# Kernel optimization log

Measured on AMD Instinct MI355X. Metric: run time of the kernel, lower is better.

## Reference

```python
import jax, jax.numpy as jnp
import numpy as np

GAMMA = 1.0
ALPHA = 0.5
EMBED_DIM = 256
N = 8192
M = 8192


def setup_inputs() -> dict:
    key = jax.random.key(0)
    k1, k2, k3, k4 = jax.random.split(key, 4)
    a = jax.random.normal(k1, (N, EMBED_DIM), dtype=jnp.float32)
    b = jax.random.normal(k2, (M, EMBED_DIM), dtype=jnp.float32)
    # torch.nn.Linear default init: U(-1/sqrt(fan_in), 1/sqrt(fan_in))
    lim = 1.0 / np.sqrt(EMBED_DIM)
    Wq = jax.random.uniform(k3, (EMBED_DIM, EMBED_DIM), jnp.float32, -lim, lim)
    Wk = jax.random.uniform(k4, (EMBED_DIM, EMBED_DIM), jnp.float32, -lim, lim)
    return {"a": a, "b": b, "Wq": Wq, "Wk": Wk}


def reference(a, b, Wq, Wk):
    # Vectorized Gram matrix of HybridKernelMethod.forward over all (a_i, b_j) pairs.
    inv_sqrt_d = np.float32(1.0 / np.sqrt(EMBED_DIM))
    ab = a @ b.T                                           # [N, M] cross dot products
    # RBF part: ||a_i - b_j||^2 = ||a_i||^2 + ||b_j||^2 - 2 a_i.b_j
    sq = (jnp.sum(a * a, axis=-1)[:, None]
          + jnp.sum(b * b, axis=-1)[None, :] - 2.0 * ab)
    rbf_sim = jnp.exp(-GAMMA * sq)                         # [N, M]
    # Attention part: per pair, q k^T is a 1x1 matrix, so softmax == 1 exactly.
    q = a @ Wq.T                                           # [N, D]
    k = b @ Wk.T                                           # [M, D]
    s = (q @ k.T) * inv_sqrt_d                             # [N, M] scores
    scores = jax.nn.softmax(s[..., None], axis=-1)[..., 0]  # all-ones, faithful to 1x1 softmax
    attn_sim = scores * ab                                 # sum((scores @ v) * x) == scores * (a.b)
    return (1.0 - ALPHA) * rbf_sim + ALPHA * attn_sim      # [N, M] Gram matrix
```

## Files before the change

kernel.cpp:

```cpp
#include <hip/hip_runtime.h>
#include <stdint.h>

#define DIM 256
#define NROWS 8192
#define OUTC 8192

#define BM 128
#define BN 128
#define BK 64

typedef __bf16 bf16x8_t __attribute__((ext_vector_type(8)));
typedef float f32x4_t __attribute__((ext_vector_type(4)));

__device__ __forceinline__ unsigned short f2bf_rne(float f) {
    unsigned int u = __float_as_uint(f);
    u += 0x7FFFu + ((u >> 16) & 1u);
    return (unsigned short)(u >> 16);
}

__global__ void prep_kernel(const float* __restrict__ src,
                            unsigned short* __restrict__ dst,
                            float* __restrict__ norms) {
    const int w = threadIdx.x >> 6;
    const int l = threadIdx.x & 63;
    const int row = blockIdx.x * 4 + w;
    const float4 v = reinterpret_cast<const float4*>(src + (size_t)row * DIM)[l];
    float ss = v.x * v.x + v.y * v.y + v.z * v.z + v.w * v.w;
#pragma unroll
    for (int off = 32; off > 0; off >>= 1) ss += __shfl_down(ss, off);
    if (l == 0) norms[row] = ss;
    ushort4 o = make_ushort4(f2bf_rne(v.x), f2bf_rne(v.y), f2bf_rne(v.z), f2bf_rne(v.w));
    reinterpret_cast<ushort4*>(dst + (size_t)row * DIM)[l] = o;
}

__global__ __launch_bounds__(256) void gemm_kernel(
        const unsigned short* __restrict__ aB,
        const unsigned short* __restrict__ bB,
        const float* __restrict__ na,
        const float* __restrict__ nb,
        float* __restrict__ out) {
    __shared__ unsigned short sA[BM * BK];
    __shared__ unsigned short sB[BN * BK];

    const int t = threadIdx.x;
    const int w = t >> 6;
    const int l = t & 63;
    const int wr = w >> 1;
    const int wc = w & 1;

    const int by = blockIdx.x >> 6;
    const int bx = blockIdx.x & 63;
    const int row0 = by * BM;
    const int col0 = bx * BN;

    f32x4_t acc[4][4];
#pragma unroll
    for (int m = 0; m < 4; ++m)
#pragma unroll
        for (int n = 0; n < 4; ++n) acc[m][n] = (f32x4_t)0.0f;

    const int lr = l >> 3;
    const int lc = (l & 7) * 8;
    const int fr = l & 15;
    const int kq = l >> 4;

#pragma unroll
    for (int kt = 0; kt < DIM / BK; ++kt) {
#pragma unroll
        for (int it = 0; it < 4; ++it) {
            const int rg = w * 4 + it;
            const int r = rg * 8 + lr;
            const unsigned short* ga = aB + (size_t)(row0 + r) * DIM + kt * BK + lc;
            const unsigned short* gb = bB + (size_t)(col0 + r) * DIM + kt * BK + lc;
            __builtin_amdgcn_global_load_lds(
                (const __attribute__((address_space(1))) void*)ga,
                (__attribute__((address_space(3))) void*)&sA[rg * 8 * BK], 16, 0, 0);
            __builtin_amdgcn_global_load_lds(
                (const __attribute__((address_space(1))) void*)gb,
                (__attribute__((address_space(3))) void*)&sB[rg * 8 * BK], 16, 0, 0);
        }
        __syncthreads();

#pragma unroll
        for (int ks = 0; ks < 2; ++ks) {
            bf16x8_t af[4], bfr[4];
#pragma unroll
            for (int m = 0; m < 4; ++m)
                af[m] = *reinterpret_cast<const bf16x8_t*>(
                    &sA[(wr * 64 + m * 16 + fr) * BK + ks * 32 + kq * 8]);
#pragma unroll
            for (int n = 0; n < 4; ++n)
                bfr[n] = *reinterpret_cast<const bf16x8_t*>(
                    &sB[(wc * 64 + n * 16 + fr) * BK + ks * 32 + kq * 8]);
#pragma unroll
            for (int m = 0; m < 4; ++m)
#pragma unroll
                for (int n = 0; n < 4; ++n)
                    acc[m][n] = __builtin_amdgcn_mfma_f32_16x16x32_bf16(
                        af[m], bfr[n], acc[m][n], 0, 0, 0);
        }
        __syncthreads();
    }

#pragma unroll
    for (int m = 0; m < 4; ++m) {
        const int rbase = row0 + wr * 64 + m * 16 + kq * 4;
#pragma unroll
        for (int q = 0; q < 4; ++q) {
            const int r = rbase + q;
            const float nar = na[r];
            const size_t ro = (size_t)r * OUTC;
#pragma unroll
            for (int n = 0; n < 4; ++n) {
                const int c = col0 + wc * 64 + n * 16 + fr;
                const float dot = acc[m][n][q];
                const float sq = nar + nb[c] - 2.0f * dot;
                out[ro + c] = 0.5f * __expf(-sq) + 0.5f * dot;
            }
        }
    }
}

__global__ void naive_kernel(const float* __restrict__ a,
                             const float* __restrict__ b,
                             float* __restrict__ out) {
    const size_t idx = (size_t)blockIdx.x * 256 + threadIdx.x;
    const int i = (int)(idx >> 13);
    const int j = (int)(idx & 8191);
    float dot = 0.f, naa = 0.f, nbb = 0.f;
    for (int k = 0; k < DIM; ++k) {
        const float x = a[(size_t)i * DIM + k];
        const float y = b[(size_t)j * DIM + k];
        dot += x * y; naa += x * x; nbb += y * y;
    }
    const float sq = naa + nbb - 2.0f * dot;
    out[idx] = 0.5f * __expf(-sq) + 0.5f * dot;
}

extern "C" void kernel_launch(void* const* d_in, const int* in_sizes, int n_in,
                              void* d_out, int out_size, void* d_ws, size_t ws_size,
                              hipStream_t stream) {
    const float* a = (const float*)d_in[0];
    const float* b = (const float*)d_in[1];
    float* out = (float*)d_out;

    const size_t bf_bytes = (size_t)NROWS * DIM * sizeof(unsigned short);
    const size_t nrm_bytes = (size_t)NROWS * sizeof(float);
    const size_t need = 2 * bf_bytes + 2 * nrm_bytes;

    if (ws_size >= need) {
        unsigned short* aBf = (unsigned short*)d_ws;
        unsigned short* bBf = (unsigned short*)((char*)d_ws + bf_bytes);
        float* na = (float*)((char*)d_ws + 2 * bf_bytes);
        float* nb = (float*)((char*)d_ws + 2 * bf_bytes + nrm_bytes);

        prep_kernel<<<NROWS / 4, 256, 0, stream>>>(a, aBf, na);
        prep_kernel<<<NROWS / 4, 256, 0, stream>>>(b, bBf, nb);
        gemm_kernel<<<(NROWS / BM) * (NROWS / BN), 256, 0, stream>>>(aBf, bBf, na, nb, out);
    } else {
        naive_kernel<<<((size_t)NROWS * NROWS) / 256, 256, 0, stream>>>(a, b, out);
    }
}
```

Measured before the change: 88.93 us.

## Persist GEMM blocks over two tiles and prefetch the next k-slice during the epilogue

Each GEMM block now handles two output tiles, and the next k-slice (or the next tile's first slice) is issued asynchronously into LDS after the compute barrier. The first slice of tile two overlaps the epilogue of tile one through a partial vmcnt wait. The two prep launches are merged into one kernel, and output stores become nontemporal to avoid polluting cache. The code relies on a hand-tuned vmcnt count and a single LDS buffer, so a wrong count could race, and the smaller grid reduces the number of waves available to hide latency.

```diff
diff --git a/kernel.cpp b/kernel.cpp
--- a/kernel.cpp
+++ b/kernel.cpp
@@ -8,6 +8,8 @@
 #define BM 128
 #define BN 128
 #define BK 64
+#define NTILES 4096
+#define GRID_GEMM 2048
 
 typedef __bf16 bf16x8_t __attribute__((ext_vector_type(8)));
 typedef float f32x4_t __attribute__((ext_vector_type(4)));
@@ -18,20 +20,48 @@
     return (unsigned short)(u >> 16);
 }
 
-__global__ void prep_kernel(const float* __restrict__ src,
-                            unsigned short* __restrict__ dst,
-                            float* __restrict__ norms) {
+__global__ void prep_kernel(const float* __restrict__ a,
+                            const float* __restrict__ b,
+                            unsigned short* __restrict__ aB,
+                            unsigned short* __restrict__ bB,
+                            float* __restrict__ na,
+                            float* __restrict__ nb) {
     const int w = threadIdx.x >> 6;
     const int l = threadIdx.x & 63;
-    const int row = blockIdx.x * 4 + w;
+    const int blk = blockIdx.x;
+    const float* src;
+    unsigned short* dst;
+    float* nrm;
+    int row;
+    if (blk < 2048) { src = a; dst = aB; nrm = na; row = blk * 4 + w; }
+    else            { src = b; dst = bB; nrm = nb; row = (blk - 2048) * 4 + w; }
     const float4 v = reinterpret_cast<const float4*>(src + (size_t)row * DIM)[l];
     float ss = v.x * v.x + v.y * v.y + v.z * v.z + v.w * v.w;
 #pragma unroll
     for (int off = 32; off > 0; off >>= 1) ss += __shfl_down(ss, off);
-    if (l == 0) norms[row] = ss;
+    if (l == 0) nrm[row] = ss;
     ushort4 o = make_ushort4(f2bf_rne(v.x), f2bf_rne(v.y), f2bf_rne(v.z), f2bf_rne(v.w));
     reinterpret_cast<ushort4*>(dst + (size_t)row * DIM)[l] = o;
 }
+
+#define STAGE(row0_, col0_, kt_)                                                 \
+    do {                                                                         \
+        _Pragma("unroll")                                                        \
+        for (int it = 0; it < 4; ++it) {                                         \
+            const int rg_ = w * 4 + it;                                          \
+            const int r_ = rg_ * 8 + lr;                                         \
+            __builtin_amdgcn_global_load_lds(                                    \
+                (const __attribute__((address_space(1))) void*)(aB +             \
+                    (size_t)((row0_) + r_) * DIM + (kt_) * BK + lc),             \
+                (__attribute__((address_space(3))) void*)&sA[rg_ * 8 * BK],      \
+                16, 0, 0);                                                       \
+            __builtin_amdgcn_global_load_lds(                                    \
+                (const __attribute__((address_space(1))) void*)(bB +             \
+                    (size_t)((col0_) + r_) * DIM + (kt_) * BK + lc),             \
+                (__attribute__((address_space(3))) void*)&sB[rg_ * 8 * BK],      \
+                16, 0, 0);                                                       \
+        }                                                                        \
+    } while (0)
 
 __global__ __launch_bounds__(256) void gemm_kernel(
         const unsigned short* __restrict__ aB,
@@ -48,76 +78,92 @@
     const int wr = w >> 1;
     const int wc = w & 1;
 
-    const int by = blockIdx.x >> 6;
-    const int bx = blockIdx.x & 63;
-    const int row0 = by * BM;
-    const int col0 = bx * BN;
-
-    f32x4_t acc[4][4];
-#pragma unroll
-    for (int m = 0; m < 4; ++m)
-#pragma unroll
-        for (int n = 0; n < 4; ++n) acc[m][n] = (f32x4_t)0.0f;
-
     const int lr = l >> 3;
     const int lc = (l & 7) * 8;
     const int fr = l & 15;
     const int kq = l >> 4;
 
-#pragma unroll
-    for (int kt = 0; kt < DIM / BK; ++kt) {
-#pragma unroll
-        for (int it = 0; it < 4; ++it) {
-            const int rg = w * 4 + it;
-            const int r = rg * 8 + lr;
-            const unsigned short* ga = aB + (size_t)(row0 + r) * DIM + kt * BK + lc;
-            const unsigned short* gb = bB + (size_t)(col0 + r) * DIM + kt * BK + lc;
-            __builtin_amdgcn_global_load_lds(
-                (const __attribute__((address_space(1))) void*)ga,
-                (__attribute__((address_space(3))) void*)&sA[rg * 8 * BK], 16, 0, 0);
-            __builtin_amdgcn_global_load_lds(
-                (const __attribute__((address_space(1))) void*)gb,
-                (__attribute__((address_space(3))) void*)&sB[rg * 8 * BK], 16, 0, 0);
+    const int bid = blockIdx.x;
+
+    {
+        const int row0 = (bid >> 6) * BM;
+        const int col0 = (bid & 63) * BN;
+        STAGE(row0, col0, 0);
+    }
+
+#pragma unroll
+    for (int ti = 0; ti < 2; ++ti) {
+        const int tile = bid + ti * GRID_GEMM;
+        const int row0 = (tile >> 6) * BM;
+        const int col0 = (tile & 63) * BN;
+
+        f32x4_t acc[4][4];
+#pragma unroll
+        for (int m = 0; m < 4; ++m)
+#pragma unroll
+            for (int n = 0; n < 4; ++n) acc[m][n] = (f32x4_t)0.0f;
+
+#pragma unroll
+        for (int kt = 0; kt < DIM / BK; ++kt) {
+            if (kt == 0 && ti > 0) {
+                asm volatile("s_waitcnt vmcnt(56)" ::: "memory");
+            } else {
+                asm volatile("s_waitcnt vmcnt(0)" ::: "memory");
+            }
+            __builtin_amdgcn_s_barrier();
+            asm volatile("" ::: "memory");
+
+#pragma unroll
+            for (int ks = 0; ks < 2; ++ks) {
+                bf16x8_t af[4], bfr[4];
+#pragma unroll
+                for (int m = 0; m < 4; ++m)
+                    af[m] = *reinterpret_cast<const bf16x8_t*>(
+                        &sA[(wr * 64 + m * 16 + fr) * BK + ks * 32 + kq * 8]);
+#pragma unroll
+                for (int n = 0; n < 4; ++n)
+                    bfr[n] = *reinterpret_cast<const bf16x8_t*>(
+                        &sB[(wc * 64 + n * 16 + fr) * BK + ks * 32 + kq * 8]);
+#pragma unroll
+                for (int m = 0; m < 4; ++m)
+#pragma unroll
+                    for (int n = 0; n < 4; ++n)
+                        acc[m][n] = __builtin_amdgcn_mfma_f32_16x16x32_bf16(
+                            af[m], bfr[n], acc[m][n], 0, 0, 0);
+            }
+
+            asm volatile("" ::: "memory");
+            __builtin_amdgcn_s_barrier();
+            asm volatile("" ::: "memory");
+
+            if (kt < DIM / BK - 1) {
+                STAGE(row0, col0, kt + 1);
+            } else if (ti == 0) {
+                const int nt_ = bid + GRID_GEMM;
+                STAGE((nt_ >> 6) * BM, (nt_ & 63) * BN, 0);
+            }
+            asm volatile("" ::: "memory");
         }
-        __syncthreads();
-
-#pragma unroll
-        for (int ks = 0; ks < 2; ++ks) {
-            bf16x8_t af[4], bfr[4];
-#pragma unroll
-            for (int m = 0; m < 4; ++m)
-                af[m] = *reinterpret_cast<const bf16x8_t*>(
-                    &sA[(wr * 64 + m * 16 + fr) * BK + ks * 32 + kq * 8]);
-#pragma unroll
-            for (int n = 0; n < 4; ++n)
-                bfr[n] = *reinterpret_cast<const bf16x8_t*>(
-                    &sB[(wc * 64 + n * 16 + fr) * BK + ks * 32 + kq * 8]);
-#pragma unroll
-            for (int m = 0; m < 4; ++m)
-#pragma unroll
-                for (int n = 0; n < 4; ++n)
-                    acc[m][n] = __builtin_amdgcn_mfma_f32_16x16x32_bf16(
-                        af[m], bfr[n], acc[m][n], 0, 0, 0);
+
+#pragma unroll
+        for (int m = 0; m < 4; ++m) {
+            const int rbase = row0 + wr * 64 + m * 16 + kq * 4;
+#pragma unroll
+            for (int q = 0; q < 4; ++q) {
+                const int r = rbase + q;
+                const float nar = na[r];
+                const size_t ro = (size_t)r * OUTC;
+#pragma unroll
+                for (int n = 0; n < 4; ++n) {
+                    const int c = col0 + wc * 64 + n * 16 + fr;
+                    const float dot = acc[m][n][q];
+                    const float sq = nar + nb[c] - 2.0f * dot;
+                    __builtin_nontemporal_store(0.5f * __expf(-sq) + 0.5f * dot,
+                                                &out[ro + c]);
+                }
+            }
         }
-        __syncthreads();
-    }
-
-#pragma unroll
-    for (int m = 0; m < 4; ++m) {
-        const int rbase = row0 + wr * 64 + m * 16 + kq * 4;
-#pragma unroll
-        for (int q = 0; q < 4; ++q) {
-            const int r = rbase + q;
-            const float nar = na[r];
-            const size_t ro = (size_t)r * OUTC;
-#pragma unroll
-            for (int n = 0; n < 4; ++n) {
-                const int c = col0 + wc * 64 + n * 16 + fr;
-                const float dot = acc[m][n][q];
-                const float sq = nar + nb[c] - 2.0f * dot;
-                out[ro + c] = 0.5f * __expf(-sq) + 0.5f * dot;
-            }
-        }
+        asm volatile("" ::: "memory");
     }
 }
 
@@ -154,9 +200,8 @@
         float* na = (float*)((char*)d_ws + 2 * bf_bytes);
         float* nb = (float*)((char*)d_ws + 2 * bf_bytes + nrm_bytes);
 
-        prep_kernel<<<NROWS / 4, 256, 0, stream>>>(a, aBf, na);
-        prep_kernel<<<NROWS / 4, 256, 0, stream>>>(b, bBf, nb);
-        gemm_kernel<<<(NROWS / BM) * (NROWS / BN), 256, 0, stream>>>(aBf, bBf, na, nb, out);
+        prep_kernel<<<4096, 256, 0, stream>>>(a, b, aBf, bBf, na, nb);
+        gemm_kernel<<<GRID_GEMM, 256, 0, stream>>>(aBf, bBf, na, nb, out);
     } else {
         naive_kernel<<<((size_t)NROWS * NROWS) / 256, 256, 0, stream>>>(a, b, out);
     }
```

After: 81.33 us. -8.5%, faster.
